# Performance work log

Hardware: AMD Instinct MI355X
Metric: run time of the kernel (lower is better)

## Reference

```python
import jax, jax.numpy as jnp
import numpy as np

MODEL_DIM = 1024
NUM_HEADS = 16
HEAD_DIM = MODEL_DIM // NUM_HEADS


def setup_inputs() -> dict:
    key = jax.random.key(0)
    ks = jax.random.split(key, 9)
    s = 1.0 / np.sqrt(MODEL_DIM)
    d = {
        "query": jax.random.normal(ks[0], (2, 2048, MODEL_DIM), dtype=jnp.float32),
        "Wq": jax.random.normal(ks[1], (MODEL_DIM, MODEL_DIM), dtype=jnp.float32) * s,
        "bq": jnp.zeros((MODEL_DIM,), dtype=jnp.float32),
        "Wk": jax.random.normal(ks[2], (MODEL_DIM, MODEL_DIM), dtype=jnp.float32) * s,
        "bk": jnp.zeros((MODEL_DIM,), dtype=jnp.float32),
        "Wv": jax.random.normal(ks[3], (MODEL_DIM, MODEL_DIM), dtype=jnp.float32) * s,
        "bv": jnp.zeros((MODEL_DIM,), dtype=jnp.float32),
        "Wo": jax.random.normal(ks[4], (MODEL_DIM, MODEL_DIM), dtype=jnp.float32) * s,
        "bo": jnp.zeros((MODEL_DIM,), dtype=jnp.float32),
    }
    return d


def reference(query, Wq, bq, Wk, bk, Wv, bv, Wo, bo):
    B, S, D = query.shape
    H, hd = NUM_HEADS, HEAD_DIM
    # self-attention: key = value = query
    q = (query @ Wq.T + bq).reshape(B, S, H, hd).transpose(0, 2, 1, 3)  # [B,H,S,hd]
    k = (query @ Wk.T + bk).reshape(B, S, H, hd).transpose(0, 2, 1, 3)
    v = (query @ Wv.T + bv).reshape(B, S, H, hd).transpose(0, 2, 1, 3)
    scores = jnp.einsum("bhqd,bhkd->bhqk", q, k) / np.sqrt(hd)  # [B,H,S,S]
    attn = jax.nn.softmax(scores, axis=-1)
    ctx = jnp.einsum("bhqk,bhkd->bhqd", attn, v)  # [B,H,S,hd]
    ctx = ctx.transpose(0, 2, 1, 3).reshape(B, S, D)
    return ctx @ Wo.T + bo
```

## Files before the change

kernel.cpp:

```cpp
#include <hip/hip_runtime.h>

typedef __attribute__((ext_vector_type(8))) __bf16 bf16x8;
typedef __attribute__((ext_vector_type(8))) unsigned short ushort8;
typedef __attribute__((ext_vector_type(4))) unsigned short ushort4v;
typedef __attribute__((ext_vector_type(4))) float f32x4;
typedef __attribute__((ext_vector_type(2))) _Float16 f16x2;
typedef __attribute__((ext_vector_type(4))) _Float16 f16x4;
typedef __attribute__((ext_vector_type(8))) _Float16 f16x8;
typedef __attribute__((ext_vector_type(2))) __fp16 fp16v2;

__device__ __forceinline__ unsigned short f2bf(float f) {
    union { float f; unsigned int u; } c; c.f = f;
    unsigned int u = c.u;
    u += 0x7fffu + ((u >> 16) & 1u);
    return (unsigned short)(u >> 16);
}

__device__ __forceinline__ void async16(const void* g, void* l) {
    __builtin_amdgcn_global_load_lds(
        (const __attribute__((address_space(1))) unsigned int*)g,
        (__attribute__((address_space(3))) unsigned int*)l, 16, 0, 0);
}

__global__ __launch_bounds__(256) void cvt_all(
    const float* __restrict__ q,  const float* __restrict__ wq,
    const float* __restrict__ wk, const float* __restrict__ wv,
    const float* __restrict__ wo,
    unsigned short* __restrict__ q_bf, unsigned short* __restrict__ wqkv,
    unsigned short* __restrict__ wo_bf, float scale_k)
{
    const int NQ = 4096 * 1024, NW = 1024 * 1024;
    int i = (blockIdx.x * 256 + threadIdx.x) * 4;
    const float* src; unsigned short* dst; float sc = 1.0f; int off;
    if (i < NQ)               { src = q;  dst = q_bf;          off = i; }
    else if (i < NQ + NW)     { src = wq; dst = wqkv;          off = i - NQ; }
    else if (i < NQ + 2 * NW) { src = wk; dst = wqkv + NW;     off = i - NQ - NW; sc = scale_k; }
    else if (i < NQ + 3 * NW) { src = wv; dst = wqkv + 2 * NW; off = i - NQ - 2 * NW; }
    else                      { src = wo; dst = wo_bf;         off = i - NQ - 3 * NW; }
    float4 v = *(const float4*)(src + off);
    ushort4v o;
    o[0] = f2bf(v.x * sc); o[1] = f2bf(v.y * sc);
    o[2] = f2bf(v.z * sc); o[3] = f2bf(v.w * sc);
    *(ushort4v*)(dst + off) = o;
}

__global__ __launch_bounds__(256) void qkv_gemm(
    const unsigned short* __restrict__ A,
    const unsigned short* __restrict__ B,
    unsigned short* __restrict__ qkv,
    _Float16* __restrict__ vtg,
    const float* __restrict__ b0, const float* __restrict__ b1, const float* __restrict__ b2,
    float s1)
{
    __shared__ __align__(16) unsigned short As[128 * 64];
    __shared__ __align__(16) unsigned short Bs[128 * 64];

    const int tid  = threadIdx.x;
    const int lane = tid & 63, wave = tid >> 6;
    const int quad = lane >> 4, l15 = lane & 15;
    const int wm = wave >> 1, wn = wave & 1;
    const int by = blockIdx.y, bx = blockIdx.x;
    const int K = 1024;

    const int srow = lane >> 3;
    const int sp   = lane & 7;
    const int scl  = sp ^ srow;
    const int sw   = l15 & 7;

    f32x4 acc[4][4];
#pragma unroll
    for (int i = 0; i < 4; ++i)
#pragma unroll
        for (int j = 0; j < 4; ++j) acc[i][j] = (f32x4)(0.0f);

    for (int kt = 0; kt < 16; ++kt) {
        __syncthreads();
#pragma unroll
        for (int j = 0; j < 4; ++j) {
            int r0 = wave * 32 + j * 8;
            async16(A + (size_t)(by * 128 + r0 + srow) * K + kt * 64 + scl * 8, &As[r0 * 64]);
            async16(B + (size_t)(bx * 128 + r0 + srow) * K + kt * 64 + scl * 8, &Bs[r0 * 64]);
        }
        __syncthreads();

#pragma unroll
        for (int kh = 0; kh < 2; ++kh) {
            bf16x8 af[4], bfr[4];
#pragma unroll
            for (int mi = 0; mi < 4; ++mi)
                af[mi] = __builtin_bit_cast(bf16x8,
                    *(const ushort8*)&As[(wm * 64 + mi * 16 + l15) * 64 + ((kh * 4 + quad) ^ sw) * 8]);
#pragma unroll
            for (int ni = 0; ni < 4; ++ni)
                bfr[ni] = __builtin_bit_cast(bf16x8,
                    *(const ushort8*)&Bs[(wn * 64 + ni * 16 + l15) * 64 + ((kh * 4 + quad) ^ sw) * 8]);
#pragma unroll
            for (int mi = 0; mi < 4; ++mi)
#pragma unroll
                for (int ni = 0; ni < 4; ++ni)
                    acc[mi][ni] = __builtin_amdgcn_mfma_f32_16x16x32_bf16(af[mi], bfr[ni], acc[mi][ni], 0, 0, 0);
        }
    }

    if (bx < 16) {
#pragma unroll
        for (int ni = 0; ni < 4; ++ni) {
            int n = bx * 128 + wn * 64 + ni * 16 + l15;
            float bias = (n < 1024) ? b0[n] : b1[n - 1024] * s1;
#pragma unroll
            for (int mi = 0; mi < 4; ++mi) {
#pragma unroll
                for (int r = 0; r < 4; ++r) {
                    int m = by * 128 + wm * 64 + mi * 16 + quad * 4 + r;
                    qkv[(size_t)m * 2048 + n] = f2bf(acc[mi][ni][r] + bias);
                }
            }
        }
    } else {
        const int mb = by * 128 + wm * 64;
        const int b  = mb >> 11;
        const int st = (mb & 2047) >> 6;
#pragma unroll
        for (int ni = 0; ni < 4; ++ni) {
            int vf = (bx - 16) * 128 + wn * 64 + ni * 16 + l15;
            int h = vf >> 6, hd = vf & 63;
            float bias = b2[vf];
            _Float16* vrow = vtg + ((size_t)((b * 16 + h) * 64 + hd)) * 2048 + st * 64;
#pragma unroll
            for (int mi = 0; mi < 4; ++mi) {
                int p = ((mi >> 1) * 4 + quad) ^ (l15 & 7);
                f16x4 o;
#pragma unroll
                for (int r = 0; r < 4; ++r) o[r] = (_Float16)(acc[mi][ni][r] + bias);
                *(f16x4*)(vrow + p * 8 + (mi & 1) * 4) = o;
            }
        }
    }
}

__global__ __launch_bounds__(256) void out_gemm(
    const unsigned short* __restrict__ A,
    const unsigned short* __restrict__ B,
    float* __restrict__ Cout,
    const float* __restrict__ bo)
{
    __shared__ __align__(16) unsigned short As[128 * 64];
    __shared__ __align__(16) unsigned short Bs[64 * 64];

    const int tid  = threadIdx.x;
    const int lane = tid & 63, wave = tid >> 6;
    const int quad = lane >> 4, l15 = lane & 15;
    const int wm = wave >> 1, wn = wave & 1;
    const int by = blockIdx.y, bx = blockIdx.x;
    const int K = 1024;

    const int srow = lane >> 3;
    const int sp   = lane & 7;
    const int scl  = sp ^ srow;
    const int sw   = l15 & 7;

    f32x4 acc[4][2];
#pragma unroll
    for (int i = 0; i < 4; ++i)
#pragma unroll
        for (int j = 0; j < 2; ++j) acc[i][j] = (f32x4)(0.0f);

    for (int kt = 0; kt < 16; ++kt) {
        __syncthreads();
#pragma unroll
        for (int j = 0; j < 4; ++j) {
            int r0 = wave * 32 + j * 8;
            async16(A + (size_t)(by * 128 + r0 + srow) * K + kt * 64 + scl * 8, &As[r0 * 64]);
        }
#pragma unroll
        for (int j = 0; j < 2; ++j) {
            int r0 = wave * 16 + j * 8;
            async16(B + (size_t)(bx * 64 + r0 + srow) * K + kt * 64 + scl * 8, &Bs[r0 * 64]);
        }
        __syncthreads();

#pragma unroll
        for (int kh = 0; kh < 2; ++kh) {
            bf16x8 af[4], bfr[2];
#pragma unroll
            for (int mi = 0; mi < 4; ++mi)
                af[mi] = __builtin_bit_cast(bf16x8,
                    *(const ushort8*)&As[(wm * 64 + mi * 16 + l15) * 64 + ((kh * 4 + quad) ^ sw) * 8]);
#pragma unroll
            for (int ni = 0; ni < 2; ++ni)
                bfr[ni] = __builtin_bit_cast(bf16x8,
                    *(const ushort8*)&Bs[(wn * 32 + ni * 16 + l15) * 64 + ((kh * 4 + quad) ^ sw) * 8]);
#pragma unroll
            for (int mi = 0; mi < 4; ++mi)
#pragma unroll
                for (int ni = 0; ni < 2; ++ni)
                    acc[mi][ni] = __builtin_amdgcn_mfma_f32_16x16x32_bf16(af[mi], bfr[ni], acc[mi][ni], 0, 0, 0);
        }
    }

#pragma unroll
    for (int ni = 0; ni < 2; ++ni) {
        int n = bx * 64 + wn * 32 + ni * 16 + l15;
        float bias = bo[n];
#pragma unroll
        for (int mi = 0; mi < 4; ++mi) {
#pragma unroll
            for (int r = 0; r < 4; ++r) {
                int m = by * 128 + wm * 64 + mi * 16 + quad * 4 + r;
                Cout[(size_t)m * 1024 + n] = acc[mi][ni][r] + bias;
            }
        }
    }
}

__global__ __launch_bounds__(256) void attn(const unsigned short* __restrict__ qkv,
                                            const _Float16* __restrict__ vtg,
                                            unsigned short* __restrict__ ctx)
{
    __shared__ __align__(16) unsigned short Ks[64 * 64];
    __shared__ __align__(16) _Float16 Vt[64 * 64];

    const int tid  = threadIdx.x;
    const int lane = tid & 63, wave = tid >> 6;
    const int quad = lane >> 4, l15 = lane & 15;
    const int bh = blockIdx.y;
    const int b = bh >> 4, h = bh & 15;
    const int q0 = blockIdx.x * 128;

    const int srow = lane >> 3;
    const int sp   = lane & 7;
    const int scl  = sp ^ srow;
    const int sw   = l15 & 7;

    bf16x8 qf[2][2];
#pragma unroll
    for (int s = 0; s < 2; ++s) {
        int qrow = b * 2048 + q0 + wave * 32 + s * 16 + l15;
#pragma unroll
        for (int kh = 0; kh < 2; ++kh)
            qf[s][kh] = __builtin_bit_cast(bf16x8,
                *(const ushort8*)(qkv + (size_t)qrow * 2048 + h * 64 + kh * 32 + quad * 8));
    }

    f32x4 ot[2][4];
#pragma unroll
    for (int s = 0; s < 2; ++s)
#pragma unroll
        for (int ht = 0; ht < 4; ++ht) ot[s][ht] = (f32x4)(0.0f);
    float l_acc[2] = {0.0f, 0.0f};
    const fp16v2 ones = {(__fp16)1.0f, (__fp16)1.0f};

    for (int kt = 0; kt < 32; ++kt) {
        __syncthreads();
#pragma unroll
        for (int i = 0; i < 2; ++i) {
            int row = i * 32 + wave * 8 + srow;
            async16(qkv + (size_t)(b * 2048 + kt * 64 + row) * 2048 + 1024 + h * 64 + scl * 8,
                    &Ks[(i * 32 + wave * 8) * 64]);
            async16(vtg + (size_t)(bh * 64 + row) * 2048 + kt * 64 + sp * 8,
                    (unsigned short*)&Vt[(i * 32 + wave * 8) * 64]);
        }
        __syncthreads();

        f16x4 pv[2][4];
#pragma unroll
        for (int mt = 0; mt < 4; ++mt) {
            const unsigned short* kb = &Ks[(mt * 16 + l15) * 64];
            bf16x8 k0 = __builtin_bit_cast(bf16x8, *(const ushort8*)(kb + (quad ^ sw) * 8));
            bf16x8 k1 = __builtin_bit_cast(bf16x8, *(const ushort8*)(kb + ((quad ^ sw) ^ 4) * 8));
#pragma unroll
            for (int s = 0; s < 2; ++s) {
                f32x4 s4 = (f32x4)(0.0f);
                s4 = __builtin_amdgcn_mfma_f32_16x16x32_bf16(k0, qf[s][0], s4, 0, 0, 0);
                s4 = __builtin_amdgcn_mfma_f32_16x16x32_bf16(k1, qf[s][1], s4, 0, 0, 0);
                float p0 = __builtin_amdgcn_exp2f(s4[0]);
                float p1 = __builtin_amdgcn_exp2f(s4[1]);
                float p2 = __builtin_amdgcn_exp2f(s4[2]);
                float p3 = __builtin_amdgcn_exp2f(s4[3]);
                fp16v2 lo = __builtin_amdgcn_cvt_pkrtz(p0, p1);
                fp16v2 hi = __builtin_amdgcn_cvt_pkrtz(p2, p3);
                l_acc[s] = __builtin_amdgcn_fdot2(lo, ones, l_acc[s], false);
                l_acc[s] = __builtin_amdgcn_fdot2(hi, ones, l_acc[s], false);
                f16x2 lo2 = __builtin_bit_cast(f16x2, lo);
                f16x2 hi2 = __builtin_bit_cast(f16x2, hi);
                pv[s][mt] = __builtin_shufflevector(lo2, hi2, 0, 1, 2, 3);
            }
        }

#pragma unroll
        for (int ht = 0; ht < 4; ++ht) {
            const _Float16* vb = &Vt[(ht * 16 + l15) * 64];
#pragma unroll
            for (int g = 0; g < 2; ++g) {
                f16x8 v8 = *(const f16x8*)(vb + (((g * 4 + quad) ^ sw)) * 8);
                f16x4 vlo = __builtin_shufflevector(v8, v8, 0, 1, 2, 3);
                f16x4 vhi = __builtin_shufflevector(v8, v8, 4, 5, 6, 7);
#pragma unroll
                for (int s = 0; s < 2; ++s) {
                    ot[s][ht] = __builtin_amdgcn_mfma_f32_16x16x16f16(vlo, pv[s][2 * g],     ot[s][ht], 0, 0, 0);
                    ot[s][ht] = __builtin_amdgcn_mfma_f32_16x16x16f16(vhi, pv[s][2 * g + 1], ot[s][ht], 0, 0, 0);
                }
            }
        }
    }

#pragma unroll
    for (int s = 0; s < 2; ++s) {
        float l = l_acc[s];
        l += __shfl_xor(l, 16, 64);
        l += __shfl_xor(l, 32, 64);
        float inv = 1.0f / l;
        int qrow = b * 2048 + q0 + wave * 32 + s * 16 + l15;
#pragma unroll
        for (int ht = 0; ht < 4; ++ht) {
            ushort4v o4;
#pragma unroll
            for (int r = 0; r < 4; ++r) o4[r] = f2bf(ot[s][ht][r] * inv);
            *(ushort4v*)(ctx + (size_t)qrow * 1024 + h * 64 + ht * 16 + quad * 4) = o4;
        }
    }
}

extern "C" void kernel_launch(void* const* d_in, const int* in_sizes, int n_in,
                              void* d_out, int out_size, void* d_ws, size_t ws_size,
                              hipStream_t stream) {
    const float* query = (const float*)d_in[0];
    const float* Wq = (const float*)d_in[1];
    const float* bq = (const float*)d_in[2];
    const float* Wk = (const float*)d_in[3];
    const float* bk = (const float*)d_in[4];
    const float* Wv = (const float*)d_in[5];
    const float* bv = (const float*)d_in[6];
    const float* Wo = (const float*)d_in[7];
    const float* bo = (const float*)d_in[8];

    char* ws = (char*)d_ws;
    unsigned short* q_bf  = (unsigned short*)(ws);
    unsigned short* ctx   = (unsigned short*)(ws);
    unsigned short* wqkv  = (unsigned short*)(ws + 8388608);
    unsigned short* wo_bf = (unsigned short*)(ws + 14680064);
    unsigned short* qkv   = (unsigned short*)(ws + 16777216);
    _Float16*       vtg   = (_Float16*)(ws + 33554432);

    const float SCALE = 0.125f * 1.4426950408889634f;

    cvt_all<<<8192, 256, 0, stream>>>(query, Wq, Wk, Wv, Wo, q_bf, wqkv, wo_bf, SCALE);
    qkv_gemm<<<dim3(24, 32), 256, 0, stream>>>(q_bf, wqkv, qkv, vtg, bq, bk, bv, SCALE);
    attn<<<dim3(16, 32), 256, 0, stream>>>(qkv, vtg, ctx);
    out_gemm<<<dim3(16, 32), 256, 0, stream>>>(ctx, wo_bf, (float*)d_out, bo);
}
```

Measured before the change: 196.9 us.

## Split attention KV range across waves with per-wave LDS and final reduction

Each block now handles 64 query rows, and its four waves each own a quarter of the key/value sequence. Each wave keeps a private LDS buffer for K and V, so the per-tile block-wide __syncthreads are gone. Partial outputs and row sums are combined through LDS at the end. This doubles the grid to 1024 blocks for better occupancy, at the cost of 64KB of LDS per block, more registers for 4 query subtiles, and a cross-wave reduction step. It also drops the overlap between waves that the shared K/V tile gave, because each wave now waits on its own loads with no double buffering.

```diff
diff --git a/kernel.cpp b/kernel.cpp
--- a/kernel.cpp
+++ b/kernel.cpp
@@ -213,63 +213,66 @@
     }
 }
 
-__global__ __launch_bounds__(256) void attn(const unsigned short* __restrict__ qkv,
-                                            const _Float16* __restrict__ vtg,
-                                            unsigned short* __restrict__ ctx)
+__global__ __launch_bounds__(256, 2) void attn(const unsigned short* __restrict__ qkv,
+                                               const _Float16* __restrict__ vtg,
+                                               unsigned short* __restrict__ ctx)
 {
-    __shared__ __align__(16) unsigned short Ks[64 * 64];
-    __shared__ __align__(16) _Float16 Vt[64 * 64];
+    __shared__ __align__(16) char smem[65536];
 
     const int tid  = threadIdx.x;
     const int lane = tid & 63, wave = tid >> 6;
     const int quad = lane >> 4, l15 = lane & 15;
     const int bh = blockIdx.y;
     const int b = bh >> 4, h = bh & 15;
-    const int q0 = blockIdx.x * 128;
+    const int q0 = blockIdx.x * 64;
 
     const int srow = lane >> 3;
     const int sp   = lane & 7;
     const int scl  = sp ^ srow;
     const int sw   = l15 & 7;
 
-    bf16x8 qf[2][2];
-#pragma unroll
-    for (int s = 0; s < 2; ++s) {
-        int qrow = b * 2048 + q0 + wave * 32 + s * 16 + l15;
+    unsigned short* KsW = (unsigned short*)(smem + wave * 16384);
+    _Float16*       VtW = (_Float16*)(smem + wave * 16384 + 8192);
+
+    bf16x8 qf[4][2];
+#pragma unroll
+    for (int s = 0; s < 4; ++s) {
+        int qrow = b * 2048 + q0 + s * 16 + l15;
 #pragma unroll
         for (int kh = 0; kh < 2; ++kh)
             qf[s][kh] = __builtin_bit_cast(bf16x8,
                 *(const ushort8*)(qkv + (size_t)qrow * 2048 + h * 64 + kh * 32 + quad * 8));
     }
 
-    f32x4 ot[2][4];
-#pragma unroll
-    for (int s = 0; s < 2; ++s)
+    f32x4 ot[4][4];
+#pragma unroll
+    for (int s = 0; s < 4; ++s)
 #pragma unroll
         for (int ht = 0; ht < 4; ++ht) ot[s][ht] = (f32x4)(0.0f);
-    float l_acc[2] = {0.0f, 0.0f};
+    float l_acc[4] = {0.0f, 0.0f, 0.0f, 0.0f};
     const fp16v2 ones = {(__fp16)1.0f, (__fp16)1.0f};
 
-    for (int kt = 0; kt < 32; ++kt) {
-        __syncthreads();
-#pragma unroll
-        for (int i = 0; i < 2; ++i) {
-            int row = i * 32 + wave * 8 + srow;
+    for (int t = 0; t < 8; ++t) {
+        int kt = wave * 8 + t;
+#pragma unroll
+        for (int j = 0; j < 8; ++j) {
+            int row = j * 8 + srow;
             async16(qkv + (size_t)(b * 2048 + kt * 64 + row) * 2048 + 1024 + h * 64 + scl * 8,
-                    &Ks[(i * 32 + wave * 8) * 64]);
+                    &KsW[j * 8 * 64]);
             async16(vtg + (size_t)(bh * 64 + row) * 2048 + kt * 64 + sp * 8,
-                    (unsigned short*)&Vt[(i * 32 + wave * 8) * 64]);
-        }
-        __syncthreads();
-
-        f16x4 pv[2][4];
+                    (unsigned short*)&VtW[j * 8 * 64]);
+        }
+        asm volatile("s_waitcnt vmcnt(0)" ::: "memory");
+        __builtin_amdgcn_sched_barrier(0);
+
+        f16x4 pv[4][4];
 #pragma unroll
         for (int mt = 0; mt < 4; ++mt) {
-            const unsigned short* kb = &Ks[(mt * 16 + l15) * 64];
+            const unsigned short* kb = &KsW[(mt * 16 + l15) * 64];
             bf16x8 k0 = __builtin_bit_cast(bf16x8, *(const ushort8*)(kb + (quad ^ sw) * 8));
             bf16x8 k1 = __builtin_bit_cast(bf16x8, *(const ushort8*)(kb + ((quad ^ sw) ^ 4) * 8));
 #pragma unroll
-            for (int s = 0; s < 2; ++s) {
+            for (int s = 0; s < 4; ++s) {
                 f32x4 s4 = (f32x4)(0.0f);
                 s4 = __builtin_amdgcn_mfma_f32_16x16x32_bf16(k0, qf[s][0], s4, 0, 0, 0);
                 s4 = __builtin_amdgcn_mfma_f32_16x16x32_bf16(k1, qf[s][1], s4, 0, 0, 0);
@@ -289,14 +292,14 @@
 
 #pragma unroll
         for (int ht = 0; ht < 4; ++ht) {
-            const _Float16* vb = &Vt[(ht * 16 + l15) * 64];
+            const _Float16* vb = &VtW[(ht * 16 + l15) * 64];
 #pragma unroll
             for (int g = 0; g < 2; ++g) {
                 f16x8 v8 = *(const f16x8*)(vb + (((g * 4 + quad) ^ sw)) * 8);
                 f16x4 vlo = __builtin_shufflevector(v8, v8, 0, 1, 2, 3);
                 f16x4 vhi = __builtin_shufflevector(v8, v8, 4, 5, 6, 7);
 #pragma unroll
-                for (int s = 0; s < 2; ++s) {
+                for (int s = 0; s < 4; ++s) {
                     ot[s][ht] = __builtin_amdgcn_mfma_f32_16x16x16f16(vlo, pv[s][2 * g],     ot[s][ht], 0, 0, 0);
                     ot[s][ht] = __builtin_amdgcn_mfma_f32_16x16x16f16(vhi, pv[s][2 * g + 1], ot[s][ht], 0, 0, 0);
                 }
@@ -304,18 +307,49 @@
         }
     }
 
-#pragma unroll
-    for (int s = 0; s < 2; ++s) {
+    float lred[4];
+#pragma unroll
+    for (int s = 0; s < 4; ++s) {
         float l = l_acc[s];
         l += __shfl_xor(l, 16, 64);
         l += __shfl_xor(l, 32, 64);
-        float inv = 1.0f / l;
-        int qrow = b * 2048 + q0 + wave * 32 + s * 16 + l15;
+        lred[s] = l;
+    }
+
+    __syncthreads();
+    float* lsh = (float*)smem;
+    if (quad == 0) {
+#pragma unroll
+        for (int s = 0; s < 4; ++s) lsh[wave * 64 + s * 16 + l15] = lred[s];
+    }
+    __syncthreads();
+    int myrow = wave * 16 + l15;
+    float lt = lsh[0 * 64 + myrow] + lsh[1 * 64 + myrow] + lsh[2 * 64 + myrow] + lsh[3 * 64 + myrow];
+    float inv = 1.0f / lt;
+
+    __syncthreads();
+    float* red = (float*)smem;
+#pragma unroll
+    for (int s = 0; s < 4; ++s) {
 #pragma unroll
         for (int ht = 0; ht < 4; ++ht) {
+            int c = (ht * 4 + quad) ^ l15;
+            *(f32x4*)(red + wave * 4096 + (s * 16 + l15) * 64 + c * 4) = ot[s][ht];
+        }
+    }
+    __syncthreads();
+    {
+        int qrow = b * 2048 + q0 + myrow;
+#pragma unroll
+        for (int ht = 0; ht < 4; ++ht) {
+            int c = (ht * 4 + quad) ^ l15;
+            f32x4 ssum = *(const f32x4*)(red + 0 * 4096 + myrow * 64 + c * 4);
+#pragma unroll
+            for (int w2 = 1; w2 < 4; ++w2)
+                ssum += *(const f32x4*)(red + w2 * 4096 + myrow * 64 + c * 4);
             ushort4v o4;
 #pragma unroll
-            for (int r = 0; r < 4; ++r) o4[r] = f2bf(ot[s][ht][r] * inv);
+            for (int r = 0; r < 4; ++r) o4[r] = f2bf(ssum[r] * inv);
             *(ushort4v*)(ctx + (size_t)qrow * 1024 + h * 64 + ht * 16 + quad * 4) = o4;
         }
     }
@@ -346,6 +380,6 @@
 
     cvt_all<<<8192, 256, 0, stream>>>(query, Wq, Wk, Wv, Wo, q_bf, wqkv, wo_bf, SCALE);
     qkv_gemm<<<dim3(24, 32), 256, 0, stream>>>(q_bf, wqkv, qkv, vtg, bq, bk, bv, SCALE);
-    attn<<<dim3(16, 32), 256, 0, stream>>>(qkv, vtg, ctx);
+    attn<<<dim3(32, 32), 256, 0, stream>>>(qkv, vtg, ctx);
     out_gemm<<<dim3(16, 32), 256, 0, stream>>>(ctx, wo_bf, (float*)d_out, bo);
 }
```

New measurement: 199.3 us. About the same (+1.2%).
